# Kernel optimization log

Hardware: AMD Instinct MI355X
Metric: run time of the kernel (lower is better)

The kernel has to match this reference:

```python
import jax, jax.numpy as jnp
import numpy as np

N = 100000      # nodes
E = 3200000     # edges
F_IN = 128      # num_features
H = 32          # hidden_dim (hard-coded in module)
C = 8           # num_classes
B = 128         # graphs in batch
BN_EPS = 1e-5


def setup_inputs() -> dict:
    key = jax.random.key(0)
    ks = jax.random.split(key, 24)
    s = 0.1
    inp = {
        "x": jax.random.normal(ks[0], (N, F_IN), jnp.float32),
        "edge_index": jax.random.randint(ks[1], (2, E), 0, N, dtype=jnp.int32),
        "batch": jnp.sort(jax.random.randint(ks[2], (N,), 0, B, dtype=jnp.int32)),
        # GINConv layer 0 (F_IN -> H -> H) MLP + BN params
        "w1_0": jax.random.normal(ks[3], (F_IN, H), jnp.float32) * s,
        "b1_0": jnp.zeros((H,), jnp.float32),
        "w2_0": jax.random.normal(ks[4], (H, H), jnp.float32) * s,
        "b2_0": jnp.zeros((H,), jnp.float32),
        "g_0": jnp.ones((H,), jnp.float32),
        "be_0": jnp.zeros((H,), jnp.float32),
        # GINConv layers 1..3 (H -> H -> H), stacked
        "w1s": jax.random.normal(ks[5], (3, H, H), jnp.float32) * s,
        "b1s": jnp.zeros((3, H), jnp.float32),
        "w2s": jax.random.normal(ks[6], (3, H, H), jnp.float32) * s,
        "b2s": jnp.zeros((3, H), jnp.float32),
        "gs": jnp.ones((3, H), jnp.float32),
        "bes": jnp.zeros((3, H), jnp.float32),
        # classifier head
        "fc1_w": jax.random.normal(ks[7], (H, H), jnp.float32) * s,
        "fc1_b": jnp.zeros((H,), jnp.float32),
        "fc2_w": jax.random.normal(ks[8], (H, C), jnp.float32) * s,
        "fc2_b": jnp.zeros((C,), jnp.float32),
    }
    return inp


def _gin_conv(h, src, dst, w1, b1, w2, b2):
    # GINConv with eps=0: MLP((1+eps)*x + sum_{j in N(i)} x_j)
    agg = jax.ops.segment_sum(h[src], dst, num_segments=N)  # scatter-add aggregation
    z = h + agg
    return jnp.maximum(z @ w1 + b1, 0.0) @ w2 + b2


def _batch_norm(h, gamma, beta):
    # BatchNorm1d in training mode: batch stats over node dim, biased variance
    mean = h.mean(axis=0)
    var = jnp.mean(jnp.square(h - mean), axis=0)
    return gamma * (h - mean) * jax.lax.rsqrt(var + BN_EPS) + beta


def reference(x, edge_index, batch, w1_0, b1_0, w2_0, b2_0, g_0, be_0,
              w1s, b1s, w2s, b2s, gs, bes, fc1_w, fc1_b, fc2_w, fc2_b):
    src, dst = edge_index[0], edge_index[1]
    h = _batch_norm(jnp.maximum(_gin_conv(x, src, dst, w1_0, b1_0, w2_0, b2_0), 0.0), g_0, be_0)
    for i in range(3):  # fixed small layer loop
        h = _batch_norm(jnp.maximum(_gin_conv(h, src, dst, w1s[i], b1s[i], w2s[i], b2s[i]), 0.0), gs[i], bes[i])
    # global_mean_pool over batch ids
    counts = jax.ops.segment_sum(jnp.ones((N,), h.dtype), batch, num_segments=B)
    pooled = jax.ops.segment_sum(h, batch, num_segments=B) / jnp.maximum(counts, 1.0)[:, None]
    h = jnp.maximum(pooled @ fc1_w + fc1_b, 0.0)
    # dropout p=0.5 treated as identity (eval-mode determinism)
    logits = h @ fc2_w + fc2_b
    return jax.nn.log_softmax(logits, axis=-1)
```

## Files before the change

kernel.cpp:

```cpp
#include <hip/hip_runtime.h>
#include <hip/hip_bf16.h>

#define NN   100000
#define EE   3200000
#define HH   32
#define BB   128
#define KMAX 96
#define LSTRIDE 97
#define NBKT 1024
#define BSPAN 98
#define EBLK 256
#define CHUNK 12500

typedef float f32x4 __attribute__((ext_vector_type(4)));

static constexpr size_t Q_OFF      = 0;
static constexpr size_t EPACK_OFF  = 6400000;
static constexpr size_t H_OFF      = 19200000;
static constexpr size_t SRC_OFF    = 32000000;
static constexpr size_t OFF_OFF    = 44800000;
static constexpr size_t HIST_OFF   = 45300000;
static constexpr size_t CUR_OFF    = 46400000;
static constexpr size_t BBASE_OFF  = 47500000;
static constexpr size_t STATS_OFF  = 47600000;
static constexpr size_t POOLED_OFF = 47601024;
static constexpr size_t PCNT_OFF   = 47617408;
static constexpr size_t ZERO_OFF   = STATS_OFF;
static constexpr size_t ZERO_BYTES = 17920;

__global__ __launch_bounds__(256) void hist_kernel(const int* __restrict__ ei,
                                                   int* __restrict__ hist) {
    __shared__ int lh[NBKT];
    int tid = threadIdx.x, blk = blockIdx.x;
    for (int i = tid; i < NBKT; i += 256) lh[i] = 0;
    __syncthreads();
    int e0 = blk * CHUNK;
    for (int e = e0 + tid; e < e0 + CHUNK; e += 256) {
        int d = ei[EE + e];
        atomicAdd(&lh[d / BSPAN], 1);
    }
    __syncthreads();
    for (int i = tid; i < NBKT; i += 256) hist[blk * NBKT + i] = lh[i];
}

__global__ __launch_bounds__(1024) void bucket_scan_kernel(const int* __restrict__ hist,
                                                           int* __restrict__ bbase,
                                                           int* __restrict__ cursor) {
    __shared__ int sm[NBKT];
    int t = threadIdx.x;
    int mine = 0;
    for (int blk = 0; blk < EBLK; blk++) mine += hist[blk * NBKT + t];
    sm[t] = mine;
    __syncthreads();
    for (int off = 1; off < NBKT; off <<= 1) {
        int v = (t >= off) ? sm[t - off] : 0;
        __syncthreads();
        sm[t] += v;
        __syncthreads();
    }
    int base = sm[t] - mine;
    bbase[t] = base;
    cursor[t] = base;
    if (t == NBKT - 1) bbase[NBKT] = sm[t];
}

__global__ __launch_bounds__(256) void scatter_kernel(const int* __restrict__ ei,
                                                      const int* __restrict__ hist,
                                                      int* __restrict__ cursor,
                                                      int* __restrict__ epack) {
    __shared__ int lbs[NBKT];
    __shared__ int lh[NBKT];
    int tid = threadIdx.x, blk = blockIdx.x;
    for (int i = tid; i < NBKT; i += 256) {
        int c = hist[blk * NBKT + i];
        lbs[i] = (c > 0) ? atomicAdd(&cursor[i], c) : 0;
        lh[i] = 0;
    }
    __syncthreads();
    int e0 = blk * CHUNK;
    for (int e = e0 + tid; e < e0 + CHUNK; e += 256) {
        int s = ei[e];
        int d = ei[EE + e];
        int b = d / BSPAN;
        int slot = lbs[b] + atomicAdd(&lh[b], 1);
        epack[slot] = s | ((d - b * BSPAN) << 17);
    }
}

__global__ __launch_bounds__(256) void csr_compact_kernel(const int* __restrict__ epack,
                                                          const int* __restrict__ bbase,
                                                          int* __restrict__ off,
                                                          int* __restrict__ srcs) {
    __shared__ int lcnt[BSPAN];
    __shared__ int lbase[BSPAN + 1];
    __shared__ int lcsr[BSPAN * LSTRIDE];
    int b = blockIdx.x;
    int base = b * BSPAN;
    int span = NN - base;
    if (span <= 0) return;
    if (span > BSPAN) span = BSPAN;
    int tid = threadIdx.x;
    for (int i = tid; i < span; i += 256) lcnt[i] = 0;
    __syncthreads();
    int p0 = bbase[b], p1 = bbase[b + 1];
    for (int i = p0 + tid; i < p1; i += 256) {
        int wd = epack[i];
        int ld = wd >> 17;
        int slot = atomicAdd(&lcnt[ld], 1);
        if (slot < KMAX) lcsr[ld * LSTRIDE + slot] = wd & 0x1FFFF;
    }
    __syncthreads();
    if (tid == 0) {
        int run = 0;
        for (int i = 0; i < span; i++) { lbase[i] = run; run += min(lcnt[i], KMAX); }
        lbase[span] = run;
    }
    __syncthreads();
    for (int i = tid; i < span; i += 256) off[base + i] = p0 + lbase[i];
    if (base + span == NN && tid == 0) off[NN] = p0 + lbase[span];
    int m = lbase[span];
    for (int j = tid; j < m; j += 256) {
        int lo = 0, hi = span - 1;
        while (lo < hi) {
            int mid = (lo + hi + 1) >> 1;
            if (lbase[mid] <= j) lo = mid; else hi = mid - 1;
        }
        srcs[p0 + j] = lcsr[lo * LSTRIDE + (j - lbase[lo])];
    }
}

__device__ __forceinline__ unsigned bf16rn(float f) {
    unsigned b = __float_as_uint(f);
    return (b + 0x7fffu + ((b >> 16) & 1u)) >> 16;
}

__device__ __forceinline__ void acc_row(float* a, uint4 v) {
    a[0] += __uint_as_float(v.x << 16);
    a[1] += __uint_as_float(v.x & 0xffff0000u);
    a[2] += __uint_as_float(v.y << 16);
    a[3] += __uint_as_float(v.y & 0xffff0000u);
    a[4] += __uint_as_float(v.z << 16);
    a[5] += __uint_as_float(v.z & 0xffff0000u);
    a[6] += __uint_as_float(v.w << 16);
    a[7] += __uint_as_float(v.w & 0xffff0000u);
}

template <int FIN>
__global__ __launch_bounds__(256) void proj_kernel(const float* __restrict__ hin,
                                                   const float* __restrict__ w1,
                                                   const float* __restrict__ stats_prev,
                                                   const float* __restrict__ gamma,
                                                   const float* __restrict__ beta,
                                                   uint4* __restrict__ q4) {
    constexpr int JC = FIN / 4;
    __shared__ float sa[32], sc[32];
    __shared__ float part[4 * 64 * 33];
    int tid = threadIdx.x;
    if constexpr (FIN == 32) {
        if (tid < 32) {
            float mean = stats_prev[tid] * (1.0f / NN);
            float var  = fmaxf(stats_prev[32 + tid] * (1.0f / NN) - mean * mean, 0.f);
            float av = gamma[tid] * rsqrtf(var + 1e-5f);
            sa[tid] = av;
            sc[tid] = beta[tid] - mean * av;
        }
        __syncthreads();
    }
    int wv = __builtin_amdgcn_readfirstlane(tid >> 6);
    int ln = tid & 63;
    int n = blockIdx.x * 64 + ln;
    float acc[32];
#pragma unroll
    for (int c = 0; c < 32; c++) acc[c] = 0.f;
    if (n < NN) {
        const float4* h4 = (const float4*)(hin + (size_t)n * FIN + wv * JC);
        float hv[JC];
#pragma unroll
        for (int k = 0; k < JC / 4; k++) {
            float4 v = h4[k];
            hv[4*k] = v.x; hv[4*k+1] = v.y; hv[4*k+2] = v.z; hv[4*k+3] = v.w;
        }
        if constexpr (FIN == 32) {
#pragma unroll
            for (int j = 0; j < JC; j++) hv[j] = fmaf(hv[j], sa[wv * JC + j], sc[wv * JC + j]);
        }
#pragma unroll 4
        for (int j = 0; j < JC; j++) {
            float hvj = hv[j];
            const float* wrow = w1 + (size_t)(wv * JC + j) * 32;
#pragma unroll
            for (int c = 0; c < 32; c++) acc[c] = fmaf(hvj, wrow[c], acc[c]);
        }
    }
    float* my = part + (wv * 64 + ln) * 33;
#pragma unroll
    for (int c = 0; c < 32; c++) my[c] = acc[c];
    __syncthreads();
    int node = tid >> 2, p = tid & 3;
    int n2 = blockIdx.x * 64 + node;
    if (n2 >= NN) return;
    float r[8];
#pragma unroll
    for (int k = 0; k < 8; k++) {
        int c = p * 8 + k;
        r[k] = (part[(0 * 64 + node) * 33 + c] + part[(1 * 64 + node) * 33 + c])
             + (part[(2 * 64 + node) * 33 + c] + part[(3 * 64 + node) * 33 + c]);
    }
    uint4 u;
    u.x = bf16rn(r[0]) | (bf16rn(r[1]) << 16);
    u.y = bf16rn(r[2]) | (bf16rn(r[3]) << 16);
    u.z = bf16rn(r[4]) | (bf16rn(r[5]) << 16);
    u.w = bf16rn(r[6]) | (bf16rn(r[7]) << 16);
    q4[(size_t)n2 * 4 + p] = u;
}

__global__ __launch_bounds__(256) void gather_mlp_kernel(const uint4* __restrict__ q4,
                                                         const int* __restrict__ srcs,
                                                         const int* __restrict__ off,
                                                         const float* __restrict__ b1,
                                                         const float* __restrict__ w2,
                                                         const float* __restrict__ b2,
                                                         float* __restrict__ hout,
                                                         float* __restrict__ stats) {
    __shared__ float w2t[32 * 33];
    __shared__ float ut[64 * 33];
    __shared__ float pst[16 * 16];
    int tid = threadIdx.x;
    for (int i = tid; i < 1024; i += 256) w2t[(i >> 5) * 33 + (i & 31)] = w2[i];
    int t = blockIdx.x * 256 + tid;
    int n = t >> 2;
    int p = tid & 3;
    int node64 = tid >> 2;
    bool valid = (n < NN);
    float a[8];
#pragma unroll
    for (int k = 0; k < 8; k++) a[k] = valid ? b1[p * 8 + k] : 0.f;
    if (valid) {
        acc_row(a, q4[(size_t)n * 4 + p]);
        int o0 = off[n];
        int d = off[n + 1] - o0;
        const int* lst = srcs + o0;
        int i = 0;
        for (; i + 8 <= d; i += 8) {
            int s0 = __builtin_nontemporal_load(lst + i);
            int s1 = __builtin_nontemporal_load(lst + i + 1);
            int s2 = __builtin_nontemporal_load(lst + i + 2);
            int s3 = __builtin_nontemporal_load(lst + i + 3);
            int s4 = __builtin_nontemporal_load(lst + i + 4);
            int s5 = __builtin_nontemporal_load(lst + i + 5);
            int s6 = __builtin_nontemporal_load(lst + i + 6);
            int s7 = __builtin_nontemporal_load(lst + i + 7);
            uint4 v0 = q4[(size_t)s0 * 4 + p];
            uint4 v1 = q4[(size_t)s1 * 4 + p];
            uint4 v2 = q4[(size_t)s2 * 4 + p];
            uint4 v3 = q4[(size_t)s3 * 4 + p];
            uint4 v4 = q4[(size_t)s4 * 4 + p];
            uint4 v5 = q4[(size_t)s5 * 4 + p];
            uint4 v6 = q4[(size_t)s6 * 4 + p];
            uint4 v7 = q4[(size_t)s7 * 4 + p];
            acc_row(a, v0); acc_row(a, v1); acc_row(a, v2); acc_row(a, v3);
            acc_row(a, v4); acc_row(a, v5); acc_row(a, v6); acc_row(a, v7);
        }
        for (; i < d; i++) {
            int s = __builtin_nontemporal_load(lst + i);
            acc_row(a, q4[(size_t)s * 4 + p]);
        }
    }
    float* urow = ut + node64 * 33 + p * 8;
#pragma unroll
    for (int k = 0; k < 8; k++) urow[k] = fmaxf(a[k], 0.f);
    __syncthreads();
    int base = p * 8;
    float o[8];
#pragma unroll
    for (int k = 0; k < 8; k++) o[k] = valid ? b2[base + k] : 0.f;
    const float* un = ut + node64 * 33;
#pragma unroll 8
    for (int j = 0; j < 32; j++) {
        float uj = un[j];
        const float* wr = w2t + j * 33 + base;
#pragma unroll
        for (int k = 0; k < 8; k++) o[k] = fmaf(uj, wr[k], o[k]);
    }
#pragma unroll
    for (int k = 0; k < 8; k++) o[k] = fmaxf(o[k], 0.f);
    if (valid) {
        f32x4 h0, h1;
        h0.x = o[0]; h0.y = o[1]; h0.z = o[2]; h0.w = o[3];
        h1.x = o[4]; h1.y = o[5]; h1.z = o[6]; h1.w = o[7];
        f32x4* hr = (f32x4*)(hout + (size_t)n * 32 + base);
        __builtin_nontemporal_store(h0, hr);
        __builtin_nontemporal_store(h1, hr + 1);
    } else {
#pragma unroll
        for (int k = 0; k < 8; k++) o[k] = 0.f;
    }
    float s[8], q[8];
#pragma unroll
    for (int k = 0; k < 8; k++) { s[k] = o[k]; q[k] = o[k] * o[k]; }
#pragma unroll
    for (int m = 4; m < 64; m <<= 1) {
#pragma unroll
        for (int k = 0; k < 8; k++) {
            s[k] += __shfl_xor(s[k], m);
            q[k] += __shfl_xor(q[k], m);
        }
    }
    int wv = tid >> 6;
    if ((tid & 63) < 4) {
        float* ps = pst + (wv * 4 + p) * 16;
#pragma unroll
        for (int k = 0; k < 8; k++) { ps[k] = s[k]; ps[8 + k] = q[k]; }
    }
    __syncthreads();
    if (tid < 64) {
        int c = tid & 31;
        int issq = tid >> 5;
        int psel = c >> 3, k = c & 7;
        float acc = 0.f;
#pragma unroll
        for (int w = 0; w < 4; w++) acc += pst[(w * 4 + psel) * 16 + issq * 8 + k];
        atomicAdd(&stats[issq * 32 + c], acc);
    }
}

#define PR 16
__global__ __launch_bounds__(256) void pool_kernel(const float* __restrict__ h,
                                                   const int* __restrict__ batch,
                                                   float* __restrict__ pooled,
                                                   float* __restrict__ pcnt) {
    int t = blockIdx.x * 256 + threadIdx.x;
    int c = t & 31;
    int g = t >> 5;
    int r0 = g * PR;
    if (r0 >= NN) return;
    int r1 = min(r0 + PR, NN);
    int cur = batch[r0];
    float acc = 0.f, cn = 0.f;
    for (int rr = r0; rr < r1; rr++) {
        int b = batch[rr];
        if (b != cur) {
            atomicAdd(&pooled[cur * 32 + c], acc);
            if (c == 0) atomicAdd(&pcnt[cur], cn);
            acc = 0.f; cn = 0.f; cur = b;
        }
        acc += h[(size_t)rr * 32 + c];
        cn += 1.f;
    }
    atomicAdd(&pooled[cur * 32 + c], acc);
    if (c == 0) atomicAdd(&pcnt[cur], cn);
}

__global__ __launch_bounds__(128) void head_kernel(const float* __restrict__ pooled,
                                                   const float* __restrict__ pcnt,
                                                   const float* __restrict__ stats3,
                                                   const float* __restrict__ g3,
                                                   const float* __restrict__ be3,
                                                   const float* __restrict__ fc1w,
                                                   const float* __restrict__ fc1b,
                                                   const float* __restrict__ fc2w,
                                                   const float* __restrict__ fc2b,
                                                   float* __restrict__ out) {
    __shared__ float sa[32], sc[32];
    int g = threadIdx.x;
    if (g < 32) {
        float mean = stats3[g] * (1.0f / NN);
        float var  = fmaxf(stats3[32 + g] * (1.0f / NN) - mean * mean, 0.f);
        float av = g3[g] * rsqrtf(var + 1e-5f);
        sa[g] = av;
        sc[g] = be3[g] - mean * av;
    }
    __syncthreads();
    if (g >= BB) return;
    float inv = 1.f / fmaxf(pcnt[g], 1.f);
    float xv[32];
#pragma unroll
    for (int c = 0; c < 32; c++) xv[c] = fmaf(sa[c], pooled[g * 32 + c] * inv, sc[c]);
    float u[32];
#pragma unroll 4
    for (int k = 0; k < 32; k++) {
        float s = fc1b[k];
#pragma unroll
        for (int c = 0; c < 32; c++) s = fmaf(xv[c], fc1w[c * 32 + k], s);
        u[k] = fmaxf(s, 0.f);
    }
    float l[8];
#pragma unroll
    for (int o = 0; o < 8; o++) {
        float s = fc2b[o];
#pragma unroll
        for (int k = 0; k < 32; k++) s = fmaf(u[k], fc2w[k * 8 + o], s);
        l[o] = s;
    }
    float m = l[0];
#pragma unroll
    for (int o = 1; o < 8; o++) m = fmaxf(m, l[o]);
    float se = 0.f;
#pragma unroll
    for (int o = 0; o < 8; o++) se += expf(l[o] - m);
    float lse = logf(se) + m;
#pragma unroll
    for (int o = 0; o < 8; o++) out[g * 8 + o] = l[o] - lse;
}

extern "C" void kernel_launch(void* const* d_in, const int* in_sizes, int n_in,
                              void* d_out, int out_size, void* d_ws, size_t ws_size,
                              hipStream_t stream) {
    const float* x    = (const float*)d_in[0];
    const int*   ei   = (const int*)d_in[1];
    const int*   batch= (const int*)d_in[2];
    const float* w1_0 = (const float*)d_in[3];
    const float* b1_0 = (const float*)d_in[4];
    const float* w2_0 = (const float*)d_in[5];
    const float* b2_0 = (const float*)d_in[6];
    const float* g_0  = (const float*)d_in[7];
    const float* be_0 = (const float*)d_in[8];
    const float* w1s  = (const float*)d_in[9];
    const float* b1s  = (const float*)d_in[10];
    const float* w2s  = (const float*)d_in[11];
    const float* b2s  = (const float*)d_in[12];
    const float* gs   = (const float*)d_in[13];
    const float* bes  = (const float*)d_in[14];
    const float* fc1w = (const float*)d_in[15];
    const float* fc1b = (const float*)d_in[16];
    const float* fc2w = (const float*)d_in[17];
    const float* fc2b = (const float*)d_in[18];
    float* out = (float*)d_out;

    char* ws = (char*)d_ws;
    uint4*    q4     = (uint4*)(ws + Q_OFF);
    int*      epack  = (int*)(ws + EPACK_OFF);
    float*    h      = (float*)(ws + H_OFF);
    int*      srcs   = (int*)(ws + SRC_OFF);
    int*      off    = (int*)(ws + OFF_OFF);
    int*      hist   = (int*)(ws + HIST_OFF);
    int*      cursor = (int*)(ws + CUR_OFF);
    int*      bbase  = (int*)(ws + BBASE_OFF);
    float*    stats  = (float*)(ws + STATS_OFF);
    float*    pooled = (float*)(ws + POOLED_OFF);
    float*    pcnt   = (float*)(ws + PCNT_OFF);

    (void)hipMemsetAsync(ws + ZERO_OFF, 0, ZERO_BYTES, stream);

    hist_kernel<<<EBLK, 256, 0, stream>>>(ei, hist);
    bucket_scan_kernel<<<1, NBKT, 0, stream>>>(hist, bbase, cursor);
    scatter_kernel<<<EBLK, 256, 0, stream>>>(ei, hist, cursor, epack);
    csr_compact_kernel<<<NBKT, 256, 0, stream>>>(epack, bbase, off, srcs);

    const int pblk = (NN + 63) / 64;
    const int gblk = (NN * 4 + 255) / 256;

    proj_kernel<128><<<pblk, 256, 0, stream>>>(x, w1_0, nullptr, nullptr, nullptr, q4);
    gather_mlp_kernel<<<gblk, 256, 0, stream>>>(q4, srcs, off, b1_0, w2_0, b2_0, h, stats);

    for (int i = 0; i < 3; i++) {
        const float* st_prev = stats + i * 64;
        proj_kernel<32><<<pblk, 256, 0, stream>>>(h, w1s + i * 1024, st_prev,
                                                  gs + i * 32, bes + i * 32, q4);
        gather_mlp_kernel<<<gblk, 256, 0, stream>>>(q4, srcs, off, b1s + i * 32,
                                                    w2s + i * 1024, b2s + i * 32, h,
                                                    stats + (i + 1) * 64);
    }

    int pthreads = ((NN + PR - 1) / PR) * 32;
    pool_kernel<<<(pthreads + 255) / 256, 256, 0, stream>>>(h, batch, pooled, pcnt);
    head_kernel<<<1, 128, 0, stream>>>(pooled, pcnt, stats + 3 * 64, gs + 2 * 32,
                                       bes + 2 * 32, fc1w, fc1b, fc2w, fc2b, out);
}
```

Measured before the change: 546.2 us.

## Replace shared-memory MLP and stats reductions with shuffles and sharded atomics

The gather MLP kernel now computes the second linear layer in registers. Each lane forms partial products for all 32 outputs from its own 8 hidden values, and two butterfly shuffle stages reduce them, replacing the shared-memory staging and barrier. The BatchNorm statistics are accumulated by per-wave global atomics into 8 sharded copies, and the readers sum the shards, which removes the block-level shared reduction. The histogram kernel also atomically accumulates bucket totals so the scan no longer loops over 256 block histograms. The cost is higher register pressure (32-float partials), more global atomics, and a larger memset.

```diff
diff --git a/kernel.cpp b/kernel.cpp
--- a/kernel.cpp
+++ b/kernel.cpp
@@ -23,13 +23,15 @@
 static constexpr size_t CUR_OFF    = 46400000;
 static constexpr size_t BBASE_OFF  = 47500000;
 static constexpr size_t STATS_OFF  = 47600000;
-static constexpr size_t POOLED_OFF = 47601024;
-static constexpr size_t PCNT_OFF   = 47617408;
+static constexpr size_t POOLED_OFF = 47608192;
+static constexpr size_t PCNT_OFF   = 47624576;
+static constexpr size_t TOTAL_OFF  = 47625088;
 static constexpr size_t ZERO_OFF   = STATS_OFF;
-static constexpr size_t ZERO_BYTES = 17920;
+static constexpr size_t ZERO_BYTES = 29184;
 
 __global__ __launch_bounds__(256) void hist_kernel(const int* __restrict__ ei,
-                                                   int* __restrict__ hist) {
+                                                   int* __restrict__ hist,
+                                                   int* __restrict__ total) {
     __shared__ int lh[NBKT];
     int tid = threadIdx.x, blk = blockIdx.x;
     for (int i = tid; i < NBKT; i += 256) lh[i] = 0;
@@ -40,16 +42,19 @@
         atomicAdd(&lh[d / BSPAN], 1);
     }
     __syncthreads();
-    for (int i = tid; i < NBKT; i += 256) hist[blk * NBKT + i] = lh[i];
-}
-
-__global__ __launch_bounds__(1024) void bucket_scan_kernel(const int* __restrict__ hist,
+    for (int i = tid; i < NBKT; i += 256) {
+        int c = lh[i];
+        hist[blk * NBKT + i] = c;
+        if (c > 0) atomicAdd(&total[i], c);
+    }
+}
+
+__global__ __launch_bounds__(1024) void bucket_scan_kernel(const int* __restrict__ total,
                                                            int* __restrict__ bbase,
                                                            int* __restrict__ cursor) {
     __shared__ int sm[NBKT];
     int t = threadIdx.x;
-    int mine = 0;
-    for (int blk = 0; blk < EBLK; blk++) mine += hist[blk * NBKT + t];
+    int mine = total[t];
     sm[t] = mine;
     __syncthreads();
     for (int off = 1; off < NBKT; off <<= 1) {
@@ -158,8 +163,14 @@
     int tid = threadIdx.x;
     if constexpr (FIN == 32) {
         if (tid < 32) {
-            float mean = stats_prev[tid] * (1.0f / NN);
-            float var  = fmaxf(stats_prev[32 + tid] * (1.0f / NN) - mean * mean, 0.f);
+            float s = 0.f, sq = 0.f;
+#pragma unroll
+            for (int k = 0; k < 8; k++) {
+                s  += stats_prev[k * 64 + tid];
+                sq += stats_prev[k * 64 + 32 + tid];
+            }
+            float mean = s * (1.0f / NN);
+            float var  = fmaxf(sq * (1.0f / NN) - mean * mean, 0.f);
             float av = gamma[tid] * rsqrtf(var + 1e-5f);
             sa[tid] = av;
             sc[tid] = beta[tid] - mean * av;
@@ -223,19 +234,19 @@
                                                          float* __restrict__ hout,
                                                          float* __restrict__ stats) {
     __shared__ float w2t[32 * 33];
-    __shared__ float ut[64 * 33];
-    __shared__ float pst[16 * 16];
     int tid = threadIdx.x;
     for (int i = tid; i < 1024; i += 256) w2t[(i >> 5) * 33 + (i & 31)] = w2[i];
+    __syncthreads();
     int t = blockIdx.x * 256 + tid;
     int n = t >> 2;
     int p = tid & 3;
-    int node64 = tid >> 2;
     bool valid = (n < NN);
     float a[8];
 #pragma unroll
-    for (int k = 0; k < 8; k++) a[k] = valid ? b1[p * 8 + k] : 0.f;
+    for (int k = 0; k < 8; k++) a[k] = 0.f;
     if (valid) {
+#pragma unroll
+        for (int k = 0; k < 8; k++) a[k] = b1[p * 8 + k];
         acc_row(a, q4[(size_t)n * 4 + p]);
         int o0 = off[n];
         int d = off[n + 1] - o0;
@@ -266,24 +277,39 @@
             acc_row(a, q4[(size_t)s * 4 + p]);
         }
     }
-    float* urow = ut + node64 * 33 + p * 8;
-#pragma unroll
-    for (int k = 0; k < 8; k++) urow[k] = fmaxf(a[k], 0.f);
-    __syncthreads();
+    float u[8];
+#pragma unroll
+    for (int k = 0; k < 8; k++) u[k] = fmaxf(a[k], 0.f);
+    float P[32];
+#pragma unroll
+    for (int c = 0; c < 32; c++) P[c] = 0.f;
+    const float* wbase = w2t + (p * 8) * 33;
+#pragma unroll
+    for (int k = 0; k < 8; k++) {
+        float uk = u[k];
+        const float* wr = wbase + k * 33;
+#pragma unroll
+        for (int c = 0; c < 32; c++) P[c] = fmaf(uk, wr[c], P[c]);
+    }
+    float Q[16];
+#pragma unroll
+    for (int r = 0; r < 16; r++) {
+        float send = (p & 2) ? P[r] : P[r + 16];
+        float recv = __shfl_xor(send, 2);
+        Q[r] = ((p & 2) ? P[r + 16] : P[r]) + recv;
+    }
+    float R[8];
+#pragma unroll
+    for (int r = 0; r < 8; r++) {
+        float send = (p & 1) ? Q[r] : Q[r + 8];
+        float recv = __shfl_xor(send, 1);
+        R[r] = ((p & 1) ? Q[r + 8] : Q[r]) + recv;
+    }
     int base = p * 8;
     float o[8];
 #pragma unroll
-    for (int k = 0; k < 8; k++) o[k] = valid ? b2[base + k] : 0.f;
-    const float* un = ut + node64 * 33;
-#pragma unroll 8
-    for (int j = 0; j < 32; j++) {
-        float uj = un[j];
-        const float* wr = w2t + j * 33 + base;
-#pragma unroll
-        for (int k = 0; k < 8; k++) o[k] = fmaf(uj, wr[k], o[k]);
-    }
-#pragma unroll
-    for (int k = 0; k < 8; k++) o[k] = fmaxf(o[k], 0.f);
+    for (int k = 0; k < 8; k++)
+        o[k] = valid ? fmaxf(R[k] + b2[base + k], 0.f) : 0.f;
     if (valid) {
         f32x4 h0, h1;
         h0.x = o[0]; h0.y = o[1]; h0.z = o[2]; h0.w = o[3];
@@ -291,9 +317,6 @@
         f32x4* hr = (f32x4*)(hout + (size_t)n * 32 + base);
         __builtin_nontemporal_store(h0, hr);
         __builtin_nontemporal_store(h1, hr + 1);
-    } else {
-#pragma unroll
-        for (int k = 0; k < 8; k++) o[k] = 0.f;
     }
     float s[8], q[8];
 #pragma unroll
@@ -306,21 +329,13 @@
             q[k] += __shfl_xor(q[k], m);
         }
     }
-    int wv = tid >> 6;
     if ((tid & 63) < 4) {
-        float* ps = pst + (wv * 4 + p) * 16;
-#pragma unroll
-        for (int k = 0; k < 8; k++) { ps[k] = s[k]; ps[8 + k] = q[k]; }
-    }
-    __syncthreads();
-    if (tid < 64) {
-        int c = tid & 31;
-        int issq = tid >> 5;
-        int psel = c >> 3, k = c & 7;
-        float acc = 0.f;
-#pragma unroll
-        for (int w = 0; w < 4; w++) acc += pst[(w * 4 + psel) * 16 + issq * 8 + k];
-        atomicAdd(&stats[issq * 32 + c], acc);
+        float* st = stats + (((blockIdx.x << 2) | (tid >> 6)) & 7) * 64;
+#pragma unroll
+        for (int k = 0; k < 8; k++) {
+            atomicAdd(&st[base + k], s[k]);
+            atomicAdd(&st[32 + base + k], q[k]);
+        }
     }
 }
 
@@ -364,8 +379,14 @@
     __shared__ float sa[32], sc[32];
     int g = threadIdx.x;
     if (g < 32) {
-        float mean = stats3[g] * (1.0f / NN);
-        float var  = fmaxf(stats3[32 + g] * (1.0f / NN) - mean * mean, 0.f);
+        float s = 0.f, sq = 0.f;
+#pragma unroll
+        for (int k = 0; k < 8; k++) {
+            s  += stats3[k * 64 + g];
+            sq += stats3[k * 64 + 32 + g];
+        }
+        float mean = s * (1.0f / NN);
+        float var  = fmaxf(sq * (1.0f / NN) - mean * mean, 0.f);
         float av = g3[g] * rsqrtf(var + 1e-5f);
         sa[g] = av;
         sc[g] = be3[g] - mean * av;
@@ -439,11 +460,12 @@
     float*    stats  = (float*)(ws + STATS_OFF);
     float*    pooled = (float*)(ws + POOLED_OFF);
     float*    pcnt   = (float*)(ws + PCNT_OFF);
+    int*      total  = (int*)(ws + TOTAL_OFF);
 
     (void)hipMemsetAsync(ws + ZERO_OFF, 0, ZERO_BYTES, stream);
 
-    hist_kernel<<<EBLK, 256, 0, stream>>>(ei, hist);
-    bucket_scan_kernel<<<1, NBKT, 0, stream>>>(hist, bbase, cursor);
+    hist_kernel<<<EBLK, 256, 0, stream>>>(ei, hist, total);
+    bucket_scan_kernel<<<1, NBKT, 0, stream>>>(total, bbase, cursor);
     scatter_kernel<<<EBLK, 256, 0, stream>>>(ei, hist, cursor, epack);
     csr_compact_kernel<<<NBKT, 256, 0, stream>>>(epack, bbase, off, srcs);
 
@@ -454,16 +476,16 @@
     gather_mlp_kernel<<<gblk, 256, 0, stream>>>(q4, srcs, off, b1_0, w2_0, b2_0, h, stats);
 
     for (int i = 0; i < 3; i++) {
-        const float* st_prev = stats + i * 64;
+        const float* st_prev = stats + i * 512;
         proj_kernel<32><<<pblk, 256, 0, stream>>>(h, w1s + i * 1024, st_prev,
                                                   gs + i * 32, bes + i * 32, q4);
         gather_mlp_kernel<<<gblk, 256, 0, stream>>>(q4, srcs, off, b1s + i * 32,
                                                     w2s + i * 1024, b2s + i * 32, h,
-                                                    stats + (i + 1) * 64);
+                                                    stats + (i + 1) * 512);
     }
 
     int pthreads = ((NN + PR - 1) / PR) * 32;
     pool_kernel<<<(pthreads + 255) / 256, 256, 0, stream>>>(h, batch, pooled, pcnt);
-    head_kernel<<<1, 128, 0, stream>>>(pooled, pcnt, stats + 3 * 64, gs + 2 * 32,
+    head_kernel<<<1, 128, 0, stream>>>(pooled, pcnt, stats + 3 * 512, gs + 2 * 32,
                                        bes + 2 * 32, fc1w, fc1b, fc2w, fc2b, out);
 }
```

New measurement: 1.054 ms. 92.9% more time.
